# Kernel optimization log

Hardware: AMD Instinct MI355X
Metric: run time of the kernel (lower is better)

## Reference

```python
import jax, jax.numpy as jnp
import numpy as np

SIGMA = 0.03   # self.sig = [0.03] in the original module
EPS = 1e-12    # guard for degenerate (zero-area) faces from random indices


def _mesh_quantities(V, F):
    """Face centers, areas (|0.5*cross|) and unit normals. V:[Nv,3], F:[Nf,3] int."""
    v0 = V[F[:, 0]]
    v1 = V[F[:, 1]]
    v2 = V[F[:, 2]]
    C = (v0 + v1 + v2) / 3.0                      # [Nf,3] face centers
    N = 0.5 * jnp.cross(v1 - v0, v2 - v0)         # [Nf,3] area-weighted normals
    L = jnp.linalg.norm(N, axis=-1)               # [Nf]  face areas
    Nn = N / jnp.maximum(L, EPS)[:, None]         # [Nf,3] unit normals
    return C, L, Nn


def _kernel_sum(Cx, Lx, Nx, Cy, Ly, Ny, gamma):
    """sum_ij Lx_i Ly_j exp(-gamma |Cx_i-Cy_j|^2) <Nx_i,Ny_j>^2  (unoriented Gauss-squared varifold kernel)."""
    d2 = (jnp.sum(Cx * Cx, -1)[:, None]
          + jnp.sum(Cy * Cy, -1)[None, :]
          - 2.0 * Cx @ Cy.T)                       # [F,F]
    dot = Nx @ Ny.T                                # [F,F]
    K = jnp.exp(-gamma * d2) * (dot * dot)
    return jnp.einsum('i,ij,j->', Lx, K, Ly)


def reference(predictions, targets, faces):
    gamma = 1.0 / (SIGMA * SIGMA)

    def per_sample(carry, xy):
        Vs, Vt = xy
        Cs, Ls, Ns = _mesh_quantities(Vs, faces)
        Ct, Lt, Nt = _mesh_quantities(Vt, faces)
        li = (_kernel_sum(Cs, Ls, Ns, Cs, Ls, Ns, gamma)
              + _kernel_sum(Ct, Lt, Nt, Ct, Lt, Nt, gamma)
              - 2.0 * _kernel_sum(Cs, Ls, Ns, Ct, Lt, Nt, gamma))
        return carry + li, None

    total, _ = jax.lax.scan(per_sample,
                            jnp.asarray(0.0, predictions.dtype),
                            (predictions, targets))
    return (total / predictions.shape[0])[None]   # shape [1], like torch.Tensor([0.0])


def setup_inputs() -> dict:
    key = jax.random.key(0)
    k1, k2, k3 = jax.random.split(key, 3)
    B, NV, NF = 4, 5023, 9976
    # scale 0.02 so inter-face distances are commensurate with sigma=0.03
    predictions = 0.02 * jax.random.normal(k1, (B, NV, 3), dtype=jnp.float32)
    targets = 0.02 * jax.random.normal(k2, (B, NV, 3), dtype=jnp.float32)
    faces = jax.random.randint(k3, (NF, 3), 0, NV, dtype=jnp.int32)
    return {"predictions": predictions, "targets": targets, "faces": faces}
```

## Files before the change

### kernel.cpp

```cpp
#include <hip/hip_runtime.h>


#define NVERT 5023
#define NFACE 9976
#define BATCH 4
#define HALFP 9984
#define NTP   (2 * HALFP)
#define NTOT  (BATCH * NTP)
#define NCH   624
#define NPAN  78
#define SPLITS 26

constexpr float GAMMA = 1.0f / (0.03f * 0.03f);
constexpr float LOG2E = 1.4426950408889634f;
constexpr float EPSV  = 1e-12f;

typedef _Float16 half8_t  __attribute__((ext_vector_type(8)));
typedef float    f32x16   __attribute__((ext_vector_type(16)));
typedef float    f32x2    __attribute__((ext_vector_type(2)));

__global__ __launch_bounds__(256)
void face_quant_kernel(const float* __restrict__ pred,
                       const float* __restrict__ targ,
                       const int*   __restrict__ faces,
                       _Float16*    __restrict__ fd,
                       float*       __restrict__ out) {
    int idx = blockIdx.x * 256 + threadIdx.x;
    if (idx == 0) out[0] = 0.0f;
    if (idx >= NTOT) return;

    int b     = idx / NTP;
    int s     = idx - b * NTP;
    int which = (s >= HALFP) ? 1 : 0;
    int f     = s - which * HALFP;

    _Float16* arec = fd + (size_t)idx * 32;
    _Float16* brec = fd + (size_t)NTOT * 32 + (size_t)idx * 32;

    if (f >= NFACE) {
        half8_t z = {};
        *(half8_t*)(arec + 0) = z; *(half8_t*)(arec + 8)  = z;
        *(half8_t*)(arec + 16) = z; *(half8_t*)(arec + 24) = z;
        *(half8_t*)(brec + 0) = z; *(half8_t*)(brec + 8)  = z;
        *(half8_t*)(brec + 16) = z; *(half8_t*)(brec + 24) = z;
        return;
    }

    const float* V = (which ? targ : pred) + (size_t)b * NVERT * 3;
    int i0 = faces[f * 3 + 0];
    int i1 = faces[f * 3 + 1];
    int i2 = faces[f * 3 + 2];

    float v0x = V[i0*3+0], v0y = V[i0*3+1], v0z = V[i0*3+2];
    float v1x = V[i1*3+0], v1y = V[i1*3+1], v1z = V[i1*3+2];
    float v2x = V[i2*3+0], v2y = V[i2*3+1], v2z = V[i2*3+2];

    const float third = 1.0f / 3.0f;
    float cx = (v0x + v1x + v2x) * third;
    float cy = (v0y + v1y + v2y) * third;
    float cz = (v0z + v1z + v2z) * third;

    float e1x = v1x - v0x, e1y = v1y - v0y, e1z = v1z - v0z;
    float e2x = v2x - v0x, e2y = v2y - v0y, e2z = v2z - v0z;

    float nx = 0.5f * (e1y * e2z - e1z * e2y);
    float ny = 0.5f * (e1z * e2x - e1x * e2z);
    float nz = 0.5f * (e1x * e2y - e1y * e2x);

    float L   = sqrtf(nx*nx + ny*ny + nz*nz);
    float inv = 1.0f / fmaxf(L, EPSV);
    float sc  = inv * sqrtf(L);
    float mx = nx * sc, my = ny * sc, mz = nz * sc;

    const float TG = 2.0f * GAMMA * LOG2E;
    float tgx = TG * cx, tgy = TG * cy, tgz = TG * cz;
    float cq  = -GAMMA * LOG2E * (cx*cx + cy*cy + cz*cz);

    _Float16 TGxh = (_Float16)tgx; _Float16 TGxl = (_Float16)(tgx - (float)TGxh);
    _Float16 TGyh = (_Float16)tgy; _Float16 TGyl = (_Float16)(tgy - (float)TGyh);
    _Float16 TGzh = (_Float16)tgz; _Float16 TGzl = (_Float16)(tgz - (float)TGzh);
    _Float16 Cxh  = (_Float16)cx;  _Float16 Cxl  = (_Float16)(cx  - (float)Cxh);
    _Float16 Cyh  = (_Float16)cy;  _Float16 Cyl  = (_Float16)(cy  - (float)Cyh);
    _Float16 Czh  = (_Float16)cz;  _Float16 Czl  = (_Float16)(cz  - (float)Czh);
    _Float16 cqh  = (_Float16)cq;  _Float16 cql  = (_Float16)(cq  - (float)cqh);
    _Float16 mxh  = (_Float16)mx;  _Float16 mxl  = (_Float16)(mx  - (float)mxh);
    _Float16 myh  = (_Float16)my;  _Float16 myl  = (_Float16)(my  - (float)myh);
    _Float16 mzh  = (_Float16)mz;  _Float16 mzl  = (_Float16)(mz  - (float)mzh);
    _Float16 one  = (_Float16)1.0f;
    _Float16 zz   = (_Float16)0.0f;

    half8_t ta0 = {TGxh, TGyh, TGzh, TGxl, TGyl, TGzl, TGxh, TGyh};
    half8_t ta1 = {TGzh, TGxl, TGyl, TGzl, cqh,  cql,  one,  one };
    half8_t da0 = {mxh,  myh,  mzh,  mxl,  myl,  mzl,  mxh,  myh };
    half8_t da1 = {mzh,  mxl,  myl,  mzl,  zz,   zz,   zz,   zz  };
    half8_t tb0 = {Cxh,  Cyh,  Czh,  Cxh,  Cyh,  Czh,  Cxl,  Cyl };
    half8_t tb1 = {Czl,  Cxl,  Cyl,  Czl,  one,  one,  cqh,  cql };
    half8_t db0 = {mxh,  myh,  mzh,  mxh,  myh,  mzh,  mxl,  myl };
    half8_t db1 = {mzl,  mxl,  myl,  mzl,  zz,   zz,   zz,   zz  };

    *(half8_t*)(arec + 0)  = ta0;  *(half8_t*)(arec + 8)  = ta1;
    *(half8_t*)(arec + 16) = da0;  *(half8_t*)(arec + 24) = da1;
    *(half8_t*)(brec + 0)  = tb0;  *(half8_t*)(brec + 8)  = tb1;
    *(half8_t*)(brec + 16) = db0;  *(half8_t*)(brec + 24) = db1;
}

__device__ __forceinline__ half8_t ld8(const _Float16* p) {
    return *(const half8_t*)p;
}

__global__ __launch_bounds__(256, 4)
void pair_sum_kernel(const _Float16* __restrict__ fd,
                     float*          __restrict__ out) {
    const int b       = blockIdx.z;
    const int pairIdx = blockIdx.x / SPLITS;
    const int s       = blockIdx.x % SPLITS;

    const _Float16* Arec = fd;
    const _Float16* Brec = fd + (size_t)NTOT * 32;

    const int lane = threadIdx.x & 63;
    const int w    = threadIdx.x >> 6;
    const int col  = lane & 31;
    const int koff = (lane >> 5) * 8;

    const size_t bface = (size_t)b * NTP;
    const size_t JSTEP = (size_t)SPLITS * 32 * 32;

    float acc = 0.0f;

    #pragma unroll 1
    for (int h = 0; h < 2; ++h) {
        const int   P  = h ? (NPAN - 1 - pairIdx) : pairIdx;
        const int   c0 = 8 * P;
        const float si = (P < NPAN / 2) ? 1.0f : -1.0f;
        const int   iters = (NCH - c0 - s + SPLITS - 1) / SPLITS;
        if (iters <= 0) continue;

        const _Float16* ap0 = Arec + (bface + (size_t)(P * 256 + w * 32 + col)) * 32 + koff;
        const _Float16* ap1 = ap0 + (size_t)128 * 32;
        half8_t aT0 = ld8(ap0);
        half8_t aD0 = ld8(ap0 + 16);
        half8_t aT1 = ld8(ap1);
        half8_t aD1 = ld8(ap1 + 16);

        const _Float16* pB = Brec + (bface + (size_t)((c0 + s) * 32 + col)) * 32 + koff;
        half8_t bT = ld8(pB);
        half8_t bD = ld8(pB + 16);

        f32x16 z = {};

        #pragma unroll 1
        for (int k = 0; k < iters; ++k) {
            const _Float16* pN = (k + 1 < iters) ? (pB + JSTEP) : pB;
            half8_t nT = ld8(pN);
            half8_t nD = ld8(pN + 16);
            pB = pN;

            f32x16 T0 = __builtin_amdgcn_mfma_f32_32x32x16_f16(aT0, bT, z, 0, 0, 0);
            f32x16 D0 = __builtin_amdgcn_mfma_f32_32x32x16_f16(aD0, bD, z, 0, 0, 0);
            f32x16 T1 = __builtin_amdgcn_mfma_f32_32x32x16_f16(aT1, bT, z, 0, 0, 0);
            f32x16 D1 = __builtin_amdgcn_mfma_f32_32x32x16_f16(aD1, bD, z, 0, 0, 0);

            f32x2 ts0 = {0.f, 0.f}, ts1 = {0.f, 0.f};
            #pragma unroll
            for (int r = 0; r < 16; r += 2) {
                f32x2 e0 = {__builtin_amdgcn_exp2f(T0[r]),
                            __builtin_amdgcn_exp2f(T0[r + 1])};
                f32x2 d0 = {D0[r], D0[r + 1]};
                d0 = d0 * d0;
                ts0 = e0 * d0 + ts0;
                f32x2 e1 = {__builtin_amdgcn_exp2f(T1[r]),
                            __builtin_amdgcn_exp2f(T1[r + 1])};
                f32x2 d1 = {D1[r], D1[r + 1]};
                d1 = d1 * d1;
                ts1 = e1 * d1 + ts1;
            }

            const int   jc  = c0 + s + SPLITS * k;
            const float sj  = (jc < NCH / 2) ? si : -si;
            const float wgt = (k == 0 && s < 8) ? 1.0f : 2.0f;
            acc = fmaf(sj * wgt, ts0.x + ts0.y + ts1.x + ts1.y, acc);

            bT = nT; bD = nD;
        }
    }

    acc *= (1.0f / BATCH);

    #pragma unroll
    for (int off = 32; off > 0; off >>= 1)
        acc += __shfl_down(acc, off, 64);

    __shared__ float wsum[4];
    if (lane == 0) wsum[w] = acc;
    __syncthreads();
    if (threadIdx.x == 0)
        atomicAdd(out, wsum[0] + wsum[1] + wsum[2] + wsum[3]);
}

extern "C" void kernel_launch(void* const* d_in, const int* in_sizes, int n_in,
                              void* d_out, int out_size, void* d_ws, size_t ws_size,
                              hipStream_t stream) {
    const float* pred  = (const float*)d_in[0];
    const float* targ  = (const float*)d_in[1];
    const int*   faces = (const int*)d_in[2];
    float*       out   = (float*)d_out;
    _Float16*    fd    = (_Float16*)d_ws;

    face_quant_kernel<<<(NTOT + 255) / 256, 256, 0, stream>>>(
        pred, targ, faces, fd, out);

    dim3 grid((NPAN / 2) * SPLITS, 1, BATCH);
    pair_sum_kernel<<<grid, 256, 0, stream>>>(fd, out);
}
```

Before: 154.9 us.

## Halve panel height, software-pipeline MFMA ahead of exp epilogue with deferred sign accumulation

Each wave now uses one 32-row A tile instead of two, and the panel count and split factor change to match (NPAN 156, SPLITS 13). The inner loop is restructured so the next tile's MFMAs are issued before the current tile's exp/square epilogue. The per-iteration sign and weight multiply is replaced by vector accumulators that are negated once when the column crosses the half boundary. The aim is to overlap matrix-core latency with the transcendental epilogue and to cut scalar work and register pressure per iteration. In exchange, each loaded B tile feeds fewer MFMAs, and the sign and weight bookkeeping is more intricate.

```diff
diff --git a/kernel.cpp b/kernel.cpp
--- a/kernel.cpp
+++ b/kernel.cpp
@@ -8,8 +8,8 @@
 #define NTP   (2 * HALFP)
 #define NTOT  (BATCH * NTP)
 #define NCH   624
-#define NPAN  78
-#define SPLITS 26
+#define NPAN  156
+#define SPLITS 13
 
 constexpr float GAMMA = 1.0f / (0.03f * 0.03f);
 constexpr float LOG2E = 1.4426950408889634f;
@@ -108,6 +108,18 @@
     return *(const half8_t*)p;
 }
 
+#define EPI(T_, D_)                                                       \
+    {                                                                     \
+        _Pragma("unroll")                                                 \
+        for (int r = 0; r < 16; r += 2) {                                 \
+            f32x2 e_ = {__builtin_amdgcn_exp2f((T_)[r]),                  \
+                        __builtin_amdgcn_exp2f((T_)[r + 1])};             \
+            f32x2 d_ = {(D_)[r], (D_)[r + 1]};                            \
+            d_ = d_ * d_;                                                 \
+            aa[(r >> 1) & 3] = e_ * d_ + aa[(r >> 1) & 3];                \
+        }                                                                 \
+    }
+
 __global__ __launch_bounds__(256, 4)
 void pair_sum_kernel(const _Float16* __restrict__ fd,
                      float*          __restrict__ out) {
@@ -127,62 +139,64 @@
     const size_t JSTEP = (size_t)SPLITS * 32 * 32;
 
     float acc = 0.0f;
+    const f32x16 z   = {};
+    const f32x2  z2  = {};
 
     #pragma unroll 1
     for (int h = 0; h < 2; ++h) {
         const int   P  = h ? (NPAN - 1 - pairIdx) : pairIdx;
-        const int   c0 = 8 * P;
+        const int   c0 = 4 * P;
         const float si = (P < NPAN / 2) ? 1.0f : -1.0f;
         const int   iters = (NCH - c0 - s + SPLITS - 1) / SPLITS;
         if (iters <= 0) continue;
 
-        const _Float16* ap0 = Arec + (bface + (size_t)(P * 256 + w * 32 + col)) * 32 + koff;
-        const _Float16* ap1 = ap0 + (size_t)128 * 32;
-        half8_t aT0 = ld8(ap0);
-        half8_t aD0 = ld8(ap0 + 16);
-        half8_t aT1 = ld8(ap1);
-        half8_t aD1 = ld8(ap1 + 16);
+        const _Float16* ap = Arec + (bface + (size_t)(P * 128 + w * 32 + col)) * 32 + koff;
+        half8_t aT = ld8(ap);
+        half8_t aD = ld8(ap + 16);
 
         const _Float16* pB = Brec + (bface + (size_t)((c0 + s) * 32 + col)) * 32 + koff;
-        half8_t bT = ld8(pB);
-        half8_t bD = ld8(pB + 16);
-
-        f32x16 z = {};
-
-        #pragma unroll 1
-        for (int k = 0; k < iters; ++k) {
-            const _Float16* pN = (k + 1 < iters) ? (pB + JSTEP) : pB;
-            half8_t nT = ld8(pN);
-            half8_t nD = ld8(pN + 16);
-            pB = pN;
-
-            f32x16 T0 = __builtin_amdgcn_mfma_f32_32x32x16_f16(aT0, bT, z, 0, 0, 0);
-            f32x16 D0 = __builtin_amdgcn_mfma_f32_32x32x16_f16(aD0, bD, z, 0, 0, 0);
-            f32x16 T1 = __builtin_amdgcn_mfma_f32_32x32x16_f16(aT1, bT, z, 0, 0, 0);
-            f32x16 D1 = __builtin_amdgcn_mfma_f32_32x32x16_f16(aD1, bD, z, 0, 0, 0);
-
-            f32x2 ts0 = {0.f, 0.f}, ts1 = {0.f, 0.f};
-            #pragma unroll
-            for (int r = 0; r < 16; r += 2) {
-                f32x2 e0 = {__builtin_amdgcn_exp2f(T0[r]),
-                            __builtin_amdgcn_exp2f(T0[r + 1])};
-                f32x2 d0 = {D0[r], D0[r + 1]};
-                d0 = d0 * d0;
-                ts0 = e0 * d0 + ts0;
-                f32x2 e1 = {__builtin_amdgcn_exp2f(T1[r]),
-                            __builtin_amdgcn_exp2f(T1[r + 1])};
-                f32x2 d1 = {D1[r], D1[r + 1]};
-                d1 = d1 * d1;
-                ts1 = e1 * d1 + ts1;
+        half8_t cT = ld8(pB), cD = ld8(pB + 16);
+
+        const int   rem   = NCH / 2 - (c0 + s);
+        const int   kc    = (rem > 0) ? ((rem + SPLITS - 1) / SPLITS) : 0;
+        const int   ktrig = (kc > 1 && kc < iters) ? kc : -1;
+        const float sgn2  = ((kc >= iters) ? si : -si) * 2.0f;
+
+        f32x2 aa[4] = {};
+
+        f32x16 T = __builtin_amdgcn_mfma_f32_32x32x16_f16(aT, cT, z, 0, 0, 0);
+        f32x16 D = __builtin_amdgcn_mfma_f32_32x32x16_f16(aD, cD, z, 0, 0, 0);
+        half8_t nT = cT, nD = cD;
+        if (iters > 1) { pB += JSTEP; nT = ld8(pB); nD = ld8(pB + 16); }
+        EPI(T, D);
+        {
+            f32x2 A2 = (aa[0] + aa[1]) + (aa[2] + aa[3]);
+            const float sj0 = (rem > 0) ? si : -si;
+            const float wg  = (s < 4) ? 1.0f : 2.0f;
+            acc = fmaf(sj0 * wg, A2.x + A2.y, acc);
+            aa[0] = z2; aa[1] = z2; aa[2] = z2; aa[3] = z2;
+        }
+
+        if (iters > 1) {
+            T = __builtin_amdgcn_mfma_f32_32x32x16_f16(aT, nT, z, 0, 0, 0);
+            D = __builtin_amdgcn_mfma_f32_32x32x16_f16(aD, nD, z, 0, 0, 0);
+            if (iters > 2) { pB += JSTEP; nT = ld8(pB); nD = ld8(pB + 16); }
+
+            #pragma unroll 2
+            for (int k = 1; k <= iters - 2; ++k) {
+                f32x16 Tn = __builtin_amdgcn_mfma_f32_32x32x16_f16(aT, nT, z, 0, 0, 0);
+                f32x16 Dn = __builtin_amdgcn_mfma_f32_32x32x16_f16(aD, nD, z, 0, 0, 0);
+                if (k + 3 <= iters) { pB += JSTEP; nT = ld8(pB); nD = ld8(pB + 16); }
+                if (k == ktrig) { aa[0] = -aa[0]; aa[1] = -aa[1]; aa[2] = -aa[2]; aa[3] = -aa[3]; }
+                EPI(T, D);
+                T = Tn; D = Dn;
             }
-
-            const int   jc  = c0 + s + SPLITS * k;
-            const float sj  = (jc < NCH / 2) ? si : -si;
-            const float wgt = (k == 0 && s < 8) ? 1.0f : 2.0f;
-            acc = fmaf(sj * wgt, ts0.x + ts0.y + ts1.x + ts1.y, acc);
-
-            bT = nT; bD = nD;
+            if (iters - 1 == ktrig) { aa[0] = -aa[0]; aa[1] = -aa[1]; aa[2] = -aa[2]; aa[3] = -aa[3]; }
+            EPI(T, D);
         }
+
+        f32x2 A2 = (aa[0] + aa[1]) + (aa[2] + aa[3]);
+        acc = fmaf(sgn2, A2.x + A2.y, acc);
     }
 
     acc *= (1.0f / BATCH);
```

After: 185.3 us. +19.7%, slower.

## Switch pair kernel to 16x16x16 MFMA tiles with software-pipelined epilogue

Applied to the files above, without the earlier changes.

Replaces the 32x32x16 MFMA tiles with 16x16x16 tiles, so each wave covers 64 A rows by 32 B columns as eight 16x16 sub-tiles. The exp2/square epilogue of each sub-tile is interleaved with the next sub-tile's MFMA, so matrix-core and vector work can overlap. Smaller accumulators cut register pressure, which lets launch bounds rise from 4 to 6 waves per SIMD. In exchange it issues more MFMA instructions, each with shorter K-utilisation per load, and more small 4-half loads.

```diff
diff --git a/kernel.cpp b/kernel.cpp
--- a/kernel.cpp
+++ b/kernel.cpp
@@ -16,7 +16,8 @@
 constexpr float EPSV  = 1e-12f;
 
 typedef _Float16 half8_t  __attribute__((ext_vector_type(8)));
-typedef float    f32x16   __attribute__((ext_vector_type(16)));
+typedef _Float16 half4_t  __attribute__((ext_vector_type(4)));
+typedef float    f32x4    __attribute__((ext_vector_type(4)));
 typedef float    f32x2    __attribute__((ext_vector_type(2)));
 
 __global__ __launch_bounds__(256)
@@ -104,11 +105,11 @@
     *(half8_t*)(brec + 16) = db0;  *(half8_t*)(brec + 24) = db1;
 }
 
-__device__ __forceinline__ half8_t ld8(const _Float16* p) {
-    return *(const half8_t*)p;
-}
-
-__global__ __launch_bounds__(256, 4)
+__device__ __forceinline__ half4_t ld4(const _Float16* p) {
+    return *(const half4_t*)p;
+}
+
+__global__ __launch_bounds__(256, 6)
 void pair_sum_kernel(const _Float16* __restrict__ fd,
                      float*          __restrict__ out) {
     const int b       = blockIdx.z;
@@ -120,8 +121,8 @@
 
     const int lane = threadIdx.x & 63;
     const int w    = threadIdx.x >> 6;
-    const int col  = lane & 31;
-    const int koff = (lane >> 5) * 8;
+    const int col  = lane & 15;
+    const int kof  = (lane >> 4) * 4;
 
     const size_t bface = (size_t)b * NTP;
     const size_t JSTEP = (size_t)SPLITS * 32 * 32;
@@ -136,52 +137,76 @@
         const int   iters = (NCH - c0 - s + SPLITS - 1) / SPLITS;
         if (iters <= 0) continue;
 
-        const _Float16* ap0 = Arec + (bface + (size_t)(P * 256 + w * 32 + col)) * 32 + koff;
-        const _Float16* ap1 = ap0 + (size_t)128 * 32;
-        half8_t aT0 = ld8(ap0);
-        half8_t aD0 = ld8(ap0 + 16);
-        half8_t aT1 = ld8(ap1);
-        half8_t aD1 = ld8(ap1 + 16);
-
-        const _Float16* pB = Brec + (bface + (size_t)((c0 + s) * 32 + col)) * 32 + koff;
-        half8_t bT = ld8(pB);
-        half8_t bD = ld8(pB + 16);
-
-        f32x16 z = {};
+        const _Float16* abase =
+            Arec + (bface + (size_t)(P * 256 + w * 64 + col)) * 32 + kof;
+        half4_t aT[4], aD[4];
+        #pragma unroll
+        for (int st = 0; st < 4; ++st) {
+            aT[st] = ld4(abase + (size_t)st * 16 * 32);
+            aD[st] = ld4(abase + (size_t)st * 16 * 32 + 16);
+        }
+
+        const _Float16* pB =
+            Brec + (bface + (size_t)((c0 + s) * 32 + col)) * 32 + kof;
+        half4_t bT0 = ld4(pB),       bD0 = ld4(pB + 16);
+        half4_t bT1 = ld4(pB + 512), bD1 = ld4(pB + 528);
+
+        const f32x4 z4 = {};
 
         #pragma unroll 1
         for (int k = 0; k < iters; ++k) {
             const _Float16* pN = (k + 1 < iters) ? (pB + JSTEP) : pB;
-            half8_t nT = ld8(pN);
-            half8_t nD = ld8(pN + 16);
+            half4_t nT0 = ld4(pN),       nD0 = ld4(pN + 16);
+            half4_t nT1 = ld4(pN + 512), nD1 = ld4(pN + 528);
             pB = pN;
 
-            f32x16 T0 = __builtin_amdgcn_mfma_f32_32x32x16_f16(aT0, bT, z, 0, 0, 0);
-            f32x16 D0 = __builtin_amdgcn_mfma_f32_32x32x16_f16(aD0, bD, z, 0, 0, 0);
-            f32x16 T1 = __builtin_amdgcn_mfma_f32_32x32x16_f16(aT1, bT, z, 0, 0, 0);
-            f32x16 D1 = __builtin_amdgcn_mfma_f32_32x32x16_f16(aD1, bD, z, 0, 0, 0);
-
-            f32x2 ts0 = {0.f, 0.f}, ts1 = {0.f, 0.f};
-            #pragma unroll
-            for (int r = 0; r < 16; r += 2) {
-                f32x2 e0 = {__builtin_amdgcn_exp2f(T0[r]),
-                            __builtin_amdgcn_exp2f(T0[r + 1])};
-                f32x2 d0 = {D0[r], D0[r + 1]};
-                d0 = d0 * d0;
-                ts0 = e0 * d0 + ts0;
-                f32x2 e1 = {__builtin_amdgcn_exp2f(T1[r]),
-                            __builtin_amdgcn_exp2f(T1[r + 1])};
-                f32x2 d1 = {D1[r], D1[r + 1]};
-                d1 = d1 * d1;
-                ts1 = e1 * d1 + ts1;
+            f32x2 aa0 = {0.f, 0.f}, aa1 = {0.f, 0.f};
+
+            f32x4 Tp = __builtin_amdgcn_mfma_f32_16x16x16f16(aT[0], bT0, z4, 0, 0, 0);
+            f32x4 Dp = __builtin_amdgcn_mfma_f32_16x16x16f16(aD[0], bD0, z4, 0, 0, 0);
+
+#define EPI4(T_, D_)                                                      \
+            {                                                             \
+                f32x2 e0_ = {__builtin_amdgcn_exp2f((T_)[0]),             \
+                             __builtin_amdgcn_exp2f((T_)[1])};            \
+                f32x2 e1_ = {__builtin_amdgcn_exp2f((T_)[2]),             \
+                             __builtin_amdgcn_exp2f((T_)[3])};            \
+                f32x2 d0_ = {(D_)[0], (D_)[1]};                           \
+                f32x2 d1_ = {(D_)[2], (D_)[3]};                           \
+                d0_ = d0_ * d0_;                                          \
+                d1_ = d1_ * d1_;                                          \
+                aa0 = e0_ * d0_ + aa0;                                    \
+                aa1 = e1_ * d1_ + aa1;                                    \
             }
+
+#define STEP(AT_, BT_, AD_, BD_)                                          \
+            {                                                             \
+                f32x4 Tc = __builtin_amdgcn_mfma_f32_16x16x16f16(         \
+                    (AT_), (BT_), z4, 0, 0, 0);                           \
+                f32x4 Dc = __builtin_amdgcn_mfma_f32_16x16x16f16(         \
+                    (AD_), (BD_), z4, 0, 0, 0);                           \
+                EPI4(Tp, Dp);                                             \
+                Tp = Tc; Dp = Dc;                                         \
+            }
+
+            STEP(aT[1], bT0, aD[1], bD0)
+            STEP(aT[2], bT0, aD[2], bD0)
+            STEP(aT[3], bT0, aD[3], bD0)
+            STEP(aT[0], bT1, aD[0], bD1)
+            STEP(aT[1], bT1, aD[1], bD1)
+            STEP(aT[2], bT1, aD[2], bD1)
+            STEP(aT[3], bT1, aD[3], bD1)
+            EPI4(Tp, Dp);
+#undef STEP
+#undef EPI4
 
             const int   jc  = c0 + s + SPLITS * k;
             const float sj  = (jc < NCH / 2) ? si : -si;
             const float wgt = (k == 0 && s < 8) ? 1.0f : 2.0f;
-            acc = fmaf(sj * wgt, ts0.x + ts0.y + ts1.x + ts1.y, acc);
-
-            bT = nT; bD = nD;
+            f32x2 A2 = aa0 + aa1;
+            acc = fmaf(sj * wgt, A2.x + A2.y, acc);
+
+            bT0 = nT0; bD0 = nD0; bT1 = nT1; bD1 = nD1;
         }
     }
 
@@ -192,7 +217,9 @@
         acc += __shfl_down(acc, off, 64);
 
     __shared__ float wsum[4];
-    if (lane == 0) wsum[w] = acc;
+    const int lane2 = threadIdx.x & 63;
+    const int w2    = threadIdx.x >> 6;
+    if (lane2 == 0) wsum[w2] = acc;
     __syncthreads();
     if (threadIdx.x == 0)
         atomicAdd(out, wsum[0] + wsum[1] + wsum[2] + wsum[3]);
```

Result: slower. 178.1 us (+15.0%).
